# Performance work log

Measured on AMD Instinct MI355X. Metric: run time of the kernel, lower is better.

Reference implementation:

```python
import jax, jax.numpy as jnp
import numpy as np

N, L, E, H = 8, 1024, 512, 4


def setup_inputs() -> dict:
    key = jax.random.key(0)
    ks = jax.random.split(key, 10)
    s = 1.0 / np.sqrt(E)
    return {
        "modalA": jax.random.normal(ks[0], (N, L, E), dtype=jnp.float32),
        "modalB": jax.random.normal(ks[1], (N, L, E), dtype=jnp.float32),
        "WqA": jax.random.normal(ks[2], (E, E), dtype=jnp.float32) * s,
        "bqA": jax.random.normal(ks[3], (E,), dtype=jnp.float32) * s,
        "WkA": jax.random.normal(ks[4], (E, E), dtype=jnp.float32) * s,
        "bkA": jax.random.normal(ks[5], (E,), dtype=jnp.float32) * s,
        "WqB": jax.random.normal(ks[6], (E, E), dtype=jnp.float32) * s,
        "bqB": jax.random.normal(ks[7], (E,), dtype=jnp.float32) * s,
        "WkB": jax.random.normal(ks[8], (E, E), dtype=jnp.float32) * s,
        "bkB": jax.random.normal(ks[9], (E,), dtype=jnp.float32) * s,
    }


def reference(modalA, modalB, WqA, bqA, WkA, bkA, WqB, bqB, WkB, bkB):
    # torch Linear: y = x @ W.T + b
    qA = modalA @ WqA.T + bqA  # [N, L, E]
    kA = modalA @ WkA.T + bkA
    qB = modalB @ WqB.T + bqB
    kB = modalB @ WkB.T + bkB

    # mean over heads of per-head dot products == full-dim dot / num_heads
    # (algebraically identical to einsum('nqhd,nkhd->nhqk').mean(1))
    inv_scale = 1.0 / (H * np.sqrt(E).astype(np.float32))

    def attn(q, k):
        scores = jnp.einsum('nqd,nkd->nqk', q, k) * inv_scale  # [N, L, L]
        return jax.nn.softmax(scores, axis=-1)

    weighted_A = attn(qA, kA)
    weighted_B = attn(qB, kB)
    weighted_AB = attn(qA, kB)
    weighted_BA = attn(qB, kA)

    cat_lower = jnp.concatenate([weighted_A, weighted_AB], axis=-1)  # [N, L, 2L]
    cat_upper = jnp.concatenate([weighted_B, weighted_BA], axis=-1)  # [N, L, 2L]
    cat = jnp.concatenate([cat_lower, cat_upper], axis=1)            # [N, 2L, 2L]
    return jnp.mean(cat, axis=0)                                     # [2L, 2L]
```

## Files before the change

### kernel.cpp

```cpp
#include <hip/hip_runtime.h>
#include <hip/hip_bf16.h>

typedef __bf16 bf16;
typedef bf16 bf16x8 __attribute__((ext_vector_type(8)));
typedef _Float16 f16;
typedef f16 f16x8 __attribute__((ext_vector_type(8)));
typedef float f32x4 __attribute__((ext_vector_type(4)));

constexpr int LL = 1024;
constexpr int EE = 512;
constexpr int NBATCH = 8;

__device__ __forceinline__ f32x4 mfma16(bf16x8 a, bf16x8 b, f32x4 c) {
    return __builtin_amdgcn_mfma_f32_16x16x32_bf16(a, b, c, 0, 0, 0);
}

#define GLOAD_LDS16(g, l)                                                     \
    __builtin_amdgcn_global_load_lds(                                         \
        (const __attribute__((address_space(1))) void*)(g),                   \
        (__attribute__((address_space(3))) void*)(l), 16, 0, 0)

__device__ __forceinline__ void wave_barrier() {
    __asm__ volatile("" ::: "memory");
    __builtin_amdgcn_s_barrier();
    __asm__ volatile("" ::: "memory");
}

constexpr int WAIT_VM6 = 0xF76;
constexpr int WAIT_VM0 = 0xF70;

struct CvtParams {
    const float* src[6];
    bf16* dst[6];
    int n8[6];
};

__global__ __launch_bounds__(256) void cvt_kernel(CvtParams p) {
    const int y = blockIdx.y;
    const float* __restrict__ src = p.src[y];
    bf16* __restrict__ dst = p.dst[y];
    const int n8 = p.n8[y];
    for (int i = blockIdx.x * 256 + threadIdx.x; i < n8; i += gridDim.x * 256) {
        float4 a = *(const float4*)(src + (size_t)i * 8);
        float4 b = *(const float4*)(src + (size_t)i * 8 + 4);
        bf16x8 o;
        o[0] = (bf16)a.x; o[1] = (bf16)a.y; o[2] = (bf16)a.z; o[3] = (bf16)a.w;
        o[4] = (bf16)b.x; o[5] = (bf16)b.y; o[6] = (bf16)b.z; o[7] = (bf16)b.w;
        *(bf16x8*)(dst + (size_t)i * 8) = o;
    }
}

struct ProjParams {
    const bf16* x[4];
    const bf16* w[4];
    const float* b[4];
};

__global__ __launch_bounds__(256, 2) void proj_kernel(ProjParams p, bf16* __restrict__ outbase) {
    const int f = blockIdx.x;
    const int xcd = f & 7;
    const int u = f >> 3;
    const int mz = xcd >> 2;
    const int by = (xcd & 3) * 16 + (u & 15);
    const int zq = (u >> 4) & 1;
    const int bxp = u >> 5;
    const int z = mz * 2 + zq;

    const bf16* __restrict__ X = p.x[z];
    const bf16* __restrict__ W = p.w[z];
    const float* __restrict__ Bv = p.b[z];
    bf16* __restrict__ O = outbase + (size_t)z * (NBATCH * LL) * EE;

    __shared__ union {
        struct { alignas(16) bf16 A[3][128][32]; alignas(16) bf16 B[3][256][32]; } st;
        alignas(16) bf16 ep[64][264];
    } sm;

    const int t = threadIdx.x;
    const int lane = t & 63, wid = t >> 6;
    const int wm = wid & 1, wn = wid >> 1;
    const int lr = lane & 15, kg = lane >> 4;

    f32x4 acc[4][8] = {};

    const int srow = t >> 2;
    const int cgl = t & 3;
    const int gcg = (cgl ^ ((srow >> 1) & 3)) * 8;
    const int scg = (kg ^ ((lr >> 1) & 3)) * 8;

    const bf16* Xrow0 = X + (size_t)(by * 128 + srow) * EE + gcg;
    const bf16* Wrow0 = W + (size_t)(bxp * 256 + srow) * EE + gcg;

    auto stage = [&](int k, int b) {
        const int k0 = k * 32;
#pragma unroll
        for (int i = 0; i < 2; ++i)
            GLOAD_LDS16(Xrow0 + (size_t)(64 * i) * EE + k0, &sm.st.A[b][srow + 64 * i][cgl * 8]);
#pragma unroll
        for (int i = 0; i < 4; ++i)
            GLOAD_LDS16(Wrow0 + (size_t)(64 * i) * EE + k0, &sm.st.B[b][srow + 64 * i][cgl * 8]);
    };
    auto compute = [&](int b) {
        bf16x8 af[4], bfr[8];
#pragma unroll
        for (int im = 0; im < 4; ++im)
            af[im] = *(const bf16x8*)&sm.st.A[b][wm * 64 + im * 16 + lr][scg];
#pragma unroll
        for (int in = 0; in < 8; ++in)
            bfr[in] = *(const bf16x8*)&sm.st.B[b][wn * 128 + in * 16 + lr][scg];
#pragma unroll
        for (int im = 0; im < 4; ++im)
#pragma unroll
            for (int in = 0; in < 8; ++in)
                acc[im][in] = mfma16(af[im], bfr[in], acc[im][in]);
    };

    stage(0, 0);
    stage(1, 1);
#pragma unroll
    for (int k = 0; k < 16; ++k) {
        if (k < 15) __builtin_amdgcn_s_waitcnt(WAIT_VM6);
        else        __builtin_amdgcn_s_waitcnt(WAIT_VM0);
        wave_barrier();
        if (k < 14) stage(k + 2, (k + 2) % 3);
        compute(k % 3);
    }
    __syncthreads();

#pragma unroll
    for (int pph = 0; pph < 2; ++pph) {
        if (wm == pph) {
#pragma unroll
            for (int im = 0; im < 4; ++im) {
                const int row = im * 16 + kg * 4;
#pragma unroll
                for (int in = 0; in < 8; ++in) {
                    const int col = wn * 128 + in * 16 + lr;
                    const float bias = Bv[bxp * 256 + col];
#pragma unroll
                    for (int r = 0; r < 4; ++r)
                        sm.ep[row + r][col] = (bf16)(acc[im][in][r] + bias);
                }
            }
        }
        __syncthreads();
#pragma unroll
        for (int i = 0; i < 8; ++i) {
            const int c = i * 256 + t;
            const int row = c >> 5, colg = (c & 31) * 8;
            *(uint4*)(O + (size_t)(by * 128 + pph * 64 + row) * EE + bxp * 256 + colg) =
                *(const uint4*)&sm.ep[row][colg];
        }
        __syncthreads();
    }
}

struct ScoresParams {
    const bf16* q[4];
    const bf16* k[4];
    f16* s[4];
};

__global__ __launch_bounds__(256, 2) void scores_kernel(ScoresParams p) {
    const int f = blockIdx.x;
    const int xcd = f & 7;
    const int j = f >> 3;
    const int z = (xcd << 2) + (j >> 5);
    const int map = z >> 3, n = z & 7;
    const int tile = j & 31;
    const int bxp = tile & 3, by = tile >> 2;

    const bf16* __restrict__ Qb = p.q[map] + (size_t)n * LL * EE;
    const bf16* __restrict__ Kb = p.k[map] + (size_t)n * LL * EE;
    f16* __restrict__ Sb = p.s[map] + (size_t)n * LL * LL;

    __shared__ union {
        struct { alignas(16) bf16 A[3][128][32]; alignas(16) bf16 B[3][256][32]; } st;
        alignas(16) f16 ep[64][264];
    } sm;

    const int t = threadIdx.x;
    const int lane = t & 63, wid = t >> 6;
    const int wm = wid & 1, wn = wid >> 1;
    const int lr = lane & 15, kg = lane >> 4;

    f32x4 acc[4][8] = {};

    const int srow = t >> 2;
    const int cgl = t & 3;
    const int gcg = (cgl ^ ((srow >> 1) & 3)) * 8;
    const int scg = (kg ^ ((lr >> 1) & 3)) * 8;

    const bf16* Qrow0 = Qb + (size_t)(by * 128 + srow) * EE + gcg;
    const bf16* Krow0 = Kb + (size_t)(bxp * 256 + srow) * EE + gcg;

    auto stage = [&](int k, int b) {
        const int k0 = k * 32;
#pragma unroll
        for (int i = 0; i < 2; ++i)
            GLOAD_LDS16(Qrow0 + (size_t)(64 * i) * EE + k0, &sm.st.A[b][srow + 64 * i][cgl * 8]);
#pragma unroll
        for (int i = 0; i < 4; ++i)
            GLOAD_LDS16(Krow0 + (size_t)(64 * i) * EE + k0, &sm.st.B[b][srow + 64 * i][cgl * 8]);
    };
    auto compute = [&](int b) {
        bf16x8 af[4], bfr[8];
#pragma unroll
        for (int im = 0; im < 4; ++im)
            af[im] = *(const bf16x8*)&sm.st.A[b][wm * 64 + im * 16 + lr][scg];
#pragma unroll
        for (int in = 0; in < 8; ++in)
            bfr[in] = *(const bf16x8*)&sm.st.B[b][wn * 128 + in * 16 + lr][scg];
#pragma unroll
        for (int im = 0; im < 4; ++im)
#pragma unroll
            for (int in = 0; in < 8; ++in)
                acc[im][in] = mfma16(af[im], bfr[in], acc[im][in]);
    };

    stage(0, 0);
    stage(1, 1);
#pragma unroll
    for (int k = 0; k < 16; ++k) {
        if (k < 15) __builtin_amdgcn_s_waitcnt(WAIT_VM6);
        else        __builtin_amdgcn_s_waitcnt(WAIT_VM0);
        wave_barrier();
        if (k < 14) stage(k + 2, (k + 2) % 3);
        compute(k % 3);
    }
    __syncthreads();

    const float inv_scale = 0.011048543456039806f;
#pragma unroll
    for (int pph = 0; pph < 2; ++pph) {
        if (wm == pph) {
#pragma unroll
            for (int im = 0; im < 4; ++im) {
                const int row = im * 16 + kg * 4;
#pragma unroll
                for (int in = 0; in < 8; ++in) {
                    const int col = wn * 128 + in * 16 + lr;
#pragma unroll
                    for (int r = 0; r < 4; ++r)
                        sm.ep[row + r][col] = (f16)(acc[im][in][r] * inv_scale);
                }
            }
        }
        __syncthreads();
#pragma unroll
        for (int i = 0; i < 8; ++i) {
            const int c = i * 256 + t;
            const int row = c >> 5, colg = (c & 31) * 8;
            *(uint4*)(Sb + (size_t)(by * 128 + pph * 64 + row) * LL + bxp * 256 + colg) =
                *(const uint4*)&sm.ep[row][colg];
        }
        __syncthreads();
    }
}

struct SmParams {
    const f16* s[4];
};

__global__ __launch_bounds__(256) void softmax_mean_kernel(SmParams p, float* __restrict__ out) {
    const int map = blockIdx.y;
    const f16* __restrict__ S = p.s[map];
    const int t = threadIdx.x;
    const int half = t >> 7;
    const int tl = t & 127;
    const int q = blockIdx.x * 2 + half;
    const int lane = t & 63, wid = t >> 6;
    __shared__ float red[NBATCH][4];

    f16x8 v[NBATCH];
#pragma unroll
    for (int n = 0; n < NBATCH; ++n)
        v[n] = *(const f16x8*)(S + ((size_t)n * LL + q) * LL + tl * 8);

    float e[NBATCH][8];
#pragma unroll
    for (int n = 0; n < NBATCH; ++n) {
        float s = 0.f;
#pragma unroll
        for (int j = 0; j < 8; ++j) {
            e[n][j] = __expf((float)v[n][j]);
            s += e[n][j];
        }
#pragma unroll
        for (int off = 32; off; off >>= 1) s += __shfl_xor(s, off);
        if (lane == 0) red[n][wid] = s;
    }
    __syncthreads();

    float acc[8] = {};
#pragma unroll
    for (int n = 0; n < NBATCH; ++n) {
        const float inv = 0.125f / (red[n][half * 2] + red[n][half * 2 + 1]);
#pragma unroll
        for (int j = 0; j < 8; ++j) acc[j] += e[n][j] * inv;
    }

    const int orow = (map >= 2 ? LL : 0) + q;
    const int ocol = (map & 1 ? LL : 0) + tl * 8;
    float* o = out + (size_t)orow * (2 * LL) + ocol;
    *(float4*)(o + 0) = make_float4(acc[0], acc[1], acc[2], acc[3]);
    *(float4*)(o + 4) = make_float4(acc[4], acc[5], acc[6], acc[7]);
}

extern "C" void kernel_launch(void* const* d_in, const int* in_sizes, int n_in,
                              void* d_out, int out_size, void* d_ws, size_t ws_size,
                              hipStream_t stream) {
    const float* modalA = (const float*)d_in[0];
    const float* modalB = (const float*)d_in[1];
    const float* WqA = (const float*)d_in[2];
    const float* bqA = (const float*)d_in[3];
    const float* WkA = (const float*)d_in[4];
    const float* bkA = (const float*)d_in[5];
    const float* WqB = (const float*)d_in[6];
    const float* bqB = (const float*)d_in[7];
    const float* WkB = (const float*)d_in[8];
    const float* bkB = (const float*)d_in[9];
    float* out = (float*)d_out;

    const size_t projN = (size_t)(NBATCH * LL) * EE;
    const size_t mapN = (size_t)NBATCH * LL * LL;
    char* base = (char*)d_ws;
    bf16* qk = (bf16*)base;
    char* region2 = base + 4 * projN * sizeof(bf16);
    bf16* XA = (bf16*)region2;
    bf16* XB = XA + projN;
    bf16* W4 = XB + projN;
    f16* S = (f16*)region2;

    CvtParams cp;
    cp.src[0] = modalA; cp.dst[0] = XA; cp.n8[0] = (int)(projN / 8);
    cp.src[1] = modalB; cp.dst[1] = XB; cp.n8[1] = (int)(projN / 8);
    const float* wsrc[4] = {WqA, WkA, WqB, WkB};
    for (int i = 0; i < 4; ++i) {
        cp.src[2 + i] = wsrc[i];
        cp.dst[2 + i] = W4 + (size_t)i * EE * EE;
        cp.n8[2 + i] = EE * EE / 8;
    }
    cvt_kernel<<<dim3(512, 6), 256, 0, stream>>>(cp);

    ProjParams pp;
    pp.x[0] = XA; pp.x[1] = XA; pp.x[2] = XB; pp.x[3] = XB;
    for (int i = 0; i < 4; ++i) pp.w[i] = W4 + (size_t)i * EE * EE;
    pp.b[0] = bqA; pp.b[1] = bkA; pp.b[2] = bqB; pp.b[3] = bkB;
    proj_kernel<<<dim3(512), 256, 0, stream>>>(pp, qk);

    const bf16* qA = qk + 0 * projN;
    const bf16* kA = qk + 1 * projN;
    const bf16* qB = qk + 2 * projN;
    const bf16* kB = qk + 3 * projN;

    ScoresParams sp;
    sp.q[0] = qA; sp.q[1] = qA; sp.q[2] = qB; sp.q[3] = qB;
    sp.k[0] = kA; sp.k[1] = kB; sp.k[2] = kB; sp.k[3] = kA;
    for (int m = 0; m < 4; ++m) sp.s[m] = S + (size_t)m * mapN;
    scores_kernel<<<dim3(1024), 256, 0, stream>>>(sp);

    SmParams smp;
    for (int m = 0; m < 4; ++m) smp.s[m] = S + (size_t)m * mapN;
    softmax_mean_kernel<<<dim3(512, 4), 256, 0, stream>>>(smp, out);
}
```

Baseline: 178.9 us.

## Fuse activation fp32-to-bf16 conversion into projection GEMM loads

```diff
diff --git a/kernel.cpp b/kernel.cpp
--- a/kernel.cpp
+++ b/kernel.cpp
@@ -30,9 +30,9 @@
 constexpr int WAIT_VM0 = 0xF70;
 
 struct CvtParams {
-    const float* src[6];
-    bf16* dst[6];
-    int n8[6];
+    const float* src[4];
+    bf16* dst[4];
+    int n8[4];
 };
 
 __global__ __launch_bounds__(256) void cvt_kernel(CvtParams p) {
@@ -51,7 +51,7 @@
 }
 
 struct ProjParams {
-    const bf16* x[4];
+    const float* x[4];
     const bf16* w[4];
     const float* b[4];
 };
@@ -66,13 +66,16 @@
     const int bxp = u >> 5;
     const int z = mz * 2 + zq;
 
-    const bf16* __restrict__ X = p.x[z];
+    const float* __restrict__ X = p.x[z];
     const bf16* __restrict__ W = p.w[z];
     const float* __restrict__ Bv = p.b[z];
     bf16* __restrict__ O = outbase + (size_t)z * (NBATCH * LL) * EE;
 
     __shared__ union {
-        struct { alignas(16) bf16 A[3][128][32]; alignas(16) bf16 B[3][256][32]; } st;
+        struct {
+            alignas(16) float Af[2][128][32];
+            alignas(16) bf16  Bs[2][256][32];
+        } st;
         alignas(16) bf16 ep[64][264];
     } sm;
 
@@ -83,31 +86,46 @@
 
     f32x4 acc[4][8] = {};
 
+    const int ar = t >> 3;
+    const int ac = t & 7;
+    const int sA = (ar >> 1) & 7;
+    const int agc = (ac ^ sA) * 4;
+    const float* Xrow0 = X + (size_t)(by * 128 + ar) * EE + agc;
+
     const int srow = t >> 2;
     const int cgl = t & 3;
     const int gcg = (cgl ^ ((srow >> 1) & 3)) * 8;
     const int scg = (kg ^ ((lr >> 1) & 3)) * 8;
-
-    const bf16* Xrow0 = X + (size_t)(by * 128 + srow) * EE + gcg;
     const bf16* Wrow0 = W + (size_t)(bxp * 256 + srow) * EE + gcg;
+
+    const int cgLo = (2 * kg) ^ ((lr >> 1) & 7);
+    const int cgHi = cgLo ^ 1;
 
     auto stage = [&](int k, int b) {
         const int k0 = k * 32;
 #pragma unroll
-        for (int i = 0; i < 2; ++i)
-            GLOAD_LDS16(Xrow0 + (size_t)(64 * i) * EE + k0, &sm.st.A[b][srow + 64 * i][cgl * 8]);
-#pragma unroll
         for (int i = 0; i < 4; ++i)
-            GLOAD_LDS16(Wrow0 + (size_t)(64 * i) * EE + k0, &sm.st.B[b][srow + 64 * i][cgl * 8]);
+            GLOAD_LDS16(Xrow0 + (size_t)(32 * i) * EE + k0, &sm.st.Af[b][32 * i + ar][ac * 4]);
+#pragma unroll
+        for (int i = 0; i < 4; ++i)
+            GLOAD_LDS16(Wrow0 + (size_t)(64 * i) * EE + k0, &sm.st.Bs[b][srow + 64 * i][cgl * 8]);
     };
     auto compute = [&](int b) {
         bf16x8 af[4], bfr[8];
 #pragma unroll
-        for (int im = 0; im < 4; ++im)
-            af[im] = *(const bf16x8*)&sm.st.A[b][wm * 64 + im * 16 + lr][scg];
+        for (int im = 0; im < 4; ++im) {
+            const int row = wm * 64 + im * 16 + lr;
+            f32x4 lo = *(const f32x4*)&sm.st.Af[b][row][cgLo * 4];
+            f32x4 hi = *(const f32x4*)&sm.st.Af[b][row][cgHi * 4];
+#pragma unroll
+            for (int e = 0; e < 4; ++e) {
+                af[im][e] = (bf16)lo[e];
+                af[im][4 + e] = (bf16)hi[e];
+            }
+        }
 #pragma unroll
         for (int in = 0; in < 8; ++in)
-            bfr[in] = *(const bf16x8*)&sm.st.B[b][wn * 128 + in * 16 + lr][scg];
+            bfr[in] = *(const bf16x8*)&sm.st.Bs[b][wn * 128 + in * 16 + lr][scg];
 #pragma unroll
         for (int im = 0; im < 4; ++im)
 #pragma unroll
@@ -116,14 +134,12 @@
     };
 
     stage(0, 0);
-    stage(1, 1);
 #pragma unroll
     for (int k = 0; k < 16; ++k) {
-        if (k < 15) __builtin_amdgcn_s_waitcnt(WAIT_VM6);
-        else        __builtin_amdgcn_s_waitcnt(WAIT_VM0);
+        __builtin_amdgcn_s_waitcnt(WAIT_VM0);
         wave_barrier();
-        if (k < 14) stage(k + 2, (k + 2) % 3);
-        compute(k % 3);
+        if (k < 15) stage(k + 1, (k + 1) & 1);
+        compute(k & 1);
     }
     __syncthreads();
 
@@ -327,24 +343,20 @@
     char* base = (char*)d_ws;
     bf16* qk = (bf16*)base;
     char* region2 = base + 4 * projN * sizeof(bf16);
-    bf16* XA = (bf16*)region2;
-    bf16* XB = XA + projN;
-    bf16* W4 = XB + projN;
+    bf16* W4 = (bf16*)region2;
     f16* S = (f16*)region2;
 
     CvtParams cp;
-    cp.src[0] = modalA; cp.dst[0] = XA; cp.n8[0] = (int)(projN / 8);
-    cp.src[1] = modalB; cp.dst[1] = XB; cp.n8[1] = (int)(projN / 8);
     const float* wsrc[4] = {WqA, WkA, WqB, WkB};
     for (int i = 0; i < 4; ++i) {
-        cp.src[2 + i] = wsrc[i];
-        cp.dst[2 + i] = W4 + (size_t)i * EE * EE;
-        cp.n8[2 + i] = EE * EE / 8;
-    }
-    cvt_kernel<<<dim3(512, 6), 256, 0, stream>>>(cp);
+        cp.src[i] = wsrc[i];
+        cp.dst[i] = W4 + (size_t)i * EE * EE;
+        cp.n8[i] = EE * EE / 8;
+    }
+    cvt_kernel<<<dim3(128, 4), 256, 0, stream>>>(cp);
 
     ProjParams pp;
-    pp.x[0] = XA; pp.x[1] = XA; pp.x[2] = XB; pp.x[3] = XB;
+    pp.x[0] = modalA; pp.x[1] = modalA; pp.x[2] = modalB; pp.x[3] = modalB;
     for (int i = 0; i < 4; ++i) pp.w[i] = W4 + (size_t)i * EE * EE;
     pp.b[0] = bqA; pp.b[1] = bkA; pp.b[2] = bqB; pp.b[3] = bkB;
     proj_kernel<<<dim3(512), 256, 0, stream>>>(pp, qk);
```

Result: faster. 170.9 us (-4.5%).
